# Kernel optimization log

Measured on AMD Instinct MI355X. Metric: run time of the kernel, lower is better.

Reference implementation:

```python
import jax, jax.numpy as jnp
import numpy as np

N_IMG, C, H_IMG, W_IMG = 6, 64, 224, 400
D_RES, H_RES, W_RES = 8, 128, 128
VOXEL = 0.4


def setup_inputs() -> dict:
    key = jax.random.key(0)
    k1, k2, k3, k4 = jax.random.split(key, 4)
    images = jax.random.normal(k1, (N_IMG, C, H_IMG, W_IMG), jnp.float32)
    fx = 0.5 * W_IMG
    K = jnp.array([[fx, 0.0, W_IMG / 2.0], [0.0, fx, H_IMG / 2.0], [0.0, 0.0, 1.0]], jnp.float32)
    intrinsic = K[None] + 0.5 * jax.random.normal(k2, (N_IMG, 3, 3), jnp.float32)
    rotation = jnp.eye(3, dtype=jnp.float32)[None] + 0.05 * jax.random.normal(k3, (N_IMG, 3, 3), jnp.float32)
    translation = 2.0 * jax.random.normal(k4, (N_IMG, 3), jnp.float32) + jnp.array([0.0, 0.0, 5.0], jnp.float32)
    return {"images": images, "intrinsic": intrinsic, "rotation": rotation,
            "translation": translation, "D": D_RES, "H": H_RES, "W": W_RES, "voxelsize": VOXEL}


def _forward(images, intrinsic, rotation, translation, D, H, W, voxelsize):
    N, Cc, Hi, Wi = images.shape
    # voxel-center grid, built exactly like torch.meshgrid(x,y,z) (ij indexing) -> [H,W,D,3]
    x = jnp.arange(H, dtype=jnp.float32) - (H - 1) / 2.0
    y = jnp.arange(W, dtype=jnp.float32) - (W - 1) / 2.0
    z = jnp.arange(D, dtype=jnp.float32) - (D - 1) / 2.0
    gx, gy, gz = jnp.meshgrid(x, y, z, indexing='ij')
    pts = jnp.stack([gx, gy, gz], axis=-1).reshape(-1, 3) * voxelsize  # [P, 3], P = H*W*D
    # lidar -> camera -> pixel (grid @ R^T + t, then @ K^T)
    cam = jnp.einsum('pj,nij->npi', pts, rotation) + translation[:, None, :]  # [N, P, 3]
    pix = jnp.einsum('npj,nij->npi', cam, intrinsic)                          # [N, P, 3]
    mask = pix[..., 2] < 0.1                                                  # [N, P]
    uv = pix[..., :2] / pix[..., 2:3]                                         # (u, v)
    g = uv[..., ::-1]                                                         # flip(-1) -> (v, u)
    scale = jnp.array([Hi - 1, Wi - 1], jnp.float32)
    g = 2.0 * g / scale - 1.0                                                 # normalized grid [N, P, 2]
    # torch grid_sample: bilinear, padding_mode='zeros', align_corners=False
    xs = ((g[..., 0] + 1.0) * Wi - 1.0) / 2.0   # grid x -> width axis
    ys = ((g[..., 1] + 1.0) * Hi - 1.0) / 2.0   # grid y -> height axis
    # clip far-out-of-range coords to keep weights finite; in-range math unchanged
    xs = jnp.clip(xs, -10.0, Wi + 10.0)
    ys = jnp.clip(ys, -10.0, Hi + 10.0)
    x0 = jnp.floor(xs)
    y0 = jnp.floor(ys)
    wx = xs - x0  # frac weights
    wy = ys - y0
    x0i = x0.astype(jnp.int32)
    y0i = y0.astype(jnp.int32)
    flat = images.reshape(N, Cc, Hi * Wi)

    def gather(ix, iy):  # ix, iy [N, P] -> [N, C, P], zeros outside image
        inr = (ix >= 0) & (ix < Wi) & (iy >= 0) & (iy < Hi)
        idx = jnp.clip(iy, 0, Hi - 1) * Wi + jnp.clip(ix, 0, Wi - 1)
        v = jax.vmap(lambda im, i: im[:, i])(flat, idx)  # [N, C, P]
        return jnp.where(inr[:, None, :], v, 0.0)

    v00 = gather(x0i, y0i)
    v10 = gather(x0i + 1, y0i)
    v01 = gather(x0i, y0i + 1)
    v11 = gather(x0i + 1, y0i + 1)
    wxe = wx[:, None, :]
    wye = wy[:, None, :]
    sampled = (v00 * (1 - wxe) * (1 - wye) + v10 * wxe * (1 - wye)
               + v01 * (1 - wxe) * wye + v11 * wxe * wye)        # [N, C, P]
    sampled = jnp.where(mask[:, None, :], 0.0, sampled)          # masked_fill
    return sampled.mean(axis=0).reshape(Cc, D, H, W)


def reference(images, intrinsic, rotation, translation, D, H, W, voxelsize):
    return _forward(images, intrinsic, rotation, translation, D, H, W, voxelsize)
```

## Files before the change

kernel.cpp:

```cpp
#include <hip/hip_runtime.h>
#include <hip/hip_fp16.h>


#define N_IMG 6
#define C_CH  64
#define HI    224
#define WI    400
#define HW    (HI * WI)
#define D_RES 8
#define H_RES 128
#define W_RES 128
#define P_TOT (D_RES * H_RES * W_RES)
#define VOX   0.4f
#define ROWH2 (WI * 32)

__global__ __launch_bounds__(256) void transpose_k(const float* __restrict__ in,
                                                   __half* __restrict__ outh) {
    __shared__ float tile[64 * 65];
    int b      = blockIdx.x;
    int n      = b / 1400;
    int s_base = (b % 1400) * 64;
    int t    = threadIdx.x;
    int col4 = t & 15;
    int crow = t >> 4;

    const float* inp = in + (size_t)n * C_CH * HW + s_base;
#pragma unroll
    for (int i = 0; i < 4; ++i) {
        int c = i * 16 + crow;
        const float4 v = *(const float4*)(inp + (size_t)c * HW + 4 * col4);
        tile[c * 65 + 4 * col4 + 0] = v.x;
        tile[c * 65 + 4 * col4 + 1] = v.y;
        tile[c * 65 + 4 * col4 + 2] = v.z;
        tile[c * 65 + 4 * col4 + 3] = v.w;
    }
    __syncthreads();

    struct __align__(8) H4 { __half2 a, b; };
    int ch4 = 4 * (t & 15);
    H4* outp = (H4*)outh;
#pragma unroll
    for (int i = 0; i < 4; ++i) {
        int pix = i * 16 + (t >> 4);
        H4 pk;
        pk.a = __floats2half2_rn(tile[(ch4 + 0) * 65 + pix],
                                 tile[(ch4 + 1) * 65 + pix]);
        pk.b = __floats2half2_rn(tile[(ch4 + 2) * 65 + pix],
                                 tile[(ch4 + 3) * 65 + pix]);
        outp[(size_t)(n * HW + s_base + pix) * 16 + (ch4 >> 2)] = pk;
    }
}

__device__ __forceinline__ void make_rec(int p, int n,
                                         const float* __restrict__ Kmat,
                                         const float* __restrict__ Rmat,
                                         const float* __restrict__ Tvec,
                                         float4& wout, int& oout) {
#pragma clang fp contract(off)
    int ih = p >> 10;
    int iw = (p >> 3) & (W_RES - 1);
    int id = p & (D_RES - 1);

    float px = ((float)ih - 63.5f) * VOX;
    float py = ((float)iw - 63.5f) * VOX;
    float pz = ((float)id - 3.5f) * VOX;

    const float* R = Rmat + n * 9;
    const float* K = Kmat + n * 9;
    const float* T = Tvec + n * 3;

    float cx = px * R[0] + py * R[1] + pz * R[2] + T[0];
    float cy = px * R[3] + py * R[4] + pz * R[5] + T[1];
    float cz = px * R[6] + py * R[7] + pz * R[8] + T[2];

    float pix0 = cx * K[0] + cy * K[1] + cz * K[2];
    float pix1 = cx * K[3] + cy * K[4] + cz * K[5];
    float pix2 = cx * K[6] + cy * K[7] + cz * K[8];

    if (pix2 < 0.1f) {
        wout = make_float4(0.0f, 0.0f, 0.0f, 0.0f);
        oout = n * (HW * 32);
        return;
    }
    float u = pix0 / pix2;
    float v = pix1 / pix2;
    float g0 = 2.0f * v / 223.0f - 1.0f;
    float g1 = 2.0f * u / 399.0f - 1.0f;
    float xs = ((g0 + 1.0f) * 400.0f - 1.0f) * 0.5f;
    float ys = ((g1 + 1.0f) * 224.0f - 1.0f) * 0.5f;
    xs = fminf(fmaxf(xs, -10.0f), 410.0f);
    ys = fminf(fmaxf(ys, -10.0f), 234.0f);
    float x0f = floorf(xs), y0f = floorf(ys);
    float wx = xs - x0f, wy = ys - y0f;
    int x0 = (int)x0f, y0 = (int)y0f;
    int x1 = x0 + 1, y1 = y0 + 1;

    int bx = min(max(x0, 0), WI - 2);
    int by = min(max(y0, 0), HI - 2);
    float wxA = (bx     == x0) ? (1.0f - wx) : ((bx     == x1) ? wx : 0.0f);
    float wxB = (bx + 1 == x0) ? (1.0f - wx) : ((bx + 1 == x1) ? wx : 0.0f);
    float wyA = (by     == y0) ? (1.0f - wy) : ((by     == y1) ? wy : 0.0f);
    float wyB = (by + 1 == y0) ? (1.0f - wy) : ((by + 1 == y1) ? wy : 0.0f);

    const float inv6 = 1.0f / 6.0f;
    wout.x = wxA * wyA * inv6;
    wout.y = wxB * wyA * inv6;
    wout.z = wxA * wyB * inv6;
    wout.w = wxB * wyB * inv6;
    oout = n * (HW * 32) + (by * WI + bx) * 32;
}

__global__ __launch_bounds__(256) void sample_k(const float* __restrict__ Kmat,
                                                const float* __restrict__ Rmat,
                                                const float* __restrict__ Tvec,
                                                const __half2* __restrict__ imgT2,
                                                float* __restrict__ out) {
    __shared__ float4 swt4[64 * N_IMG];
    __shared__ int    sof[64 * N_IMG];
    __shared__ float  sout[64 * 66];

    int t = threadIdx.x;
    int bid    = ((blockIdx.x & 7) << 8) | (blockIdx.x >> 3);
    int p_base = bid * 64;

    for (int i = t; i < 64 * N_IMG; i += 256) {
        float4 w; int o;
        make_rec(p_base + i / N_IMG, i % N_IMG, Kmat, Rmat, Tvec, w, o);
        swt4[i] = w;
        sof[i]  = o;
    }
    __syncthreads();

    int lane = t & 63;
    int wv   = t >> 6;
    int k    = lane & 31;
    int row  = lane >> 5;
    int sel  = row * 2 + (k >> 4);

    struct __align__(8) H2X2 { __half2 a, b; };
    const float*   swtF    = (const float*)swt4;
    const __half2* rowbase = imgT2 + row * ROWH2 + 2 * k;

#pragma unroll 4
    for (int j = 0; j < 16; ++j) {
        int pl = wv * 16 + j;
        float4 acc = make_float4(0.0f, 0.0f, 0.0f, 0.0f);
#pragma unroll
        for (int n = 0; n < N_IMG; ++n) {
            int   rec = pl * N_IMG + n;
            float w   = swtF[rec * 4 + sel];
            int   o   = sof[rec];
            const H2X2 v = *(const H2X2*)(rowbase + o);
            float2 lo = __half22float2(v.a);
            float2 hi = __half22float2(v.b);
            acc.x = fmaf(w, lo.x, acc.x);
            acc.y = fmaf(w, lo.y, acc.y);
            acc.z = fmaf(w, hi.x, acc.z);
            acc.w = fmaf(w, hi.y, acc.w);
        }
        acc.x += __shfl_xor(acc.x, 32, 64);
        acc.y += __shfl_xor(acc.y, 32, 64);
        acc.z += __shfl_xor(acc.z, 32, 64);
        acc.w += __shfl_xor(acc.w, 32, 64);
        acc.x += __shfl_xor(acc.x, 16, 64);
        acc.y += __shfl_xor(acc.y, 16, 64);
        acc.z += __shfl_xor(acc.z, 16, 64);
        acc.w += __shfl_xor(acc.w, 16, 64);
        if (lane < 16) {
            *(float2*)&sout[pl * 66 + 4 * lane]     = make_float2(acc.x, acc.y);
            *(float2*)&sout[pl * 66 + 4 * lane + 2] = make_float2(acc.z, acc.w);
        }
    }
    __syncthreads();

    int csub = t >> 6;
#pragma unroll
    for (int i = 0; i < 16; ++i) {
        int c = csub * 16 + i;
        __builtin_nontemporal_store(sout[lane * 66 + c],
                                    &out[(size_t)c * P_TOT + p_base + lane]);
    }
}

extern "C" void kernel_launch(void* const* d_in, const int* in_sizes, int n_in,
                              void* d_out, int out_size, void* d_ws, size_t ws_size,
                              hipStream_t stream) {
    const float* images = (const float*)d_in[0];
    const float* intr   = (const float*)d_in[1];
    const float* rot    = (const float*)d_in[2];
    const float* trans  = (const float*)d_in[3];

    __half* imgT = (__half*)d_ws;
    float*  outp = (float*)d_out;

    transpose_k<<<N_IMG * (HW / 64), 256, 0, stream>>>(images, imgT);
    sample_k<<<P_TOT / 64, 256, 0, stream>>>(intr, rot, trans,
                                             (const __half2*)imgT, outp);
}
```

Before: 259.9 us.

## Widen transpose tiles, convert to half before LDS, add XOR swizzle and XCD remap

The transpose kernel now handles 256 pixels per block instead of 64. It converts fp32 to half while loading and stores packed half4 into a 32 KB LDS tile with an XOR swizzle in place of padding. The write-out unpacks pairs of pixels into two 64-bit stores, and block IDs are remapped so each XCD gets a contiguous chunk. The goal is to cut LDS traffic and bank conflicts and improve the locality of global reads and writes in the preprocessing pass. The cost is more LDS per block, which can lower occupancy, plus extra bit manipulation.

```diff
diff --git a/kernel.cpp b/kernel.cpp
--- a/kernel.cpp
+++ b/kernel.cpp
@@ -14,40 +14,60 @@
 #define VOX   0.4f
 #define ROWH2 (WI * 32)
 
+#define TPPB  256
+#define NTILE (HW / TPPB)
+#define NTB   (N_IMG * NTILE)
+
 __global__ __launch_bounds__(256) void transpose_k(const float* __restrict__ in,
                                                    __half* __restrict__ outh) {
-    __shared__ float tile[64 * 65];
-    int b      = blockIdx.x;
-    int n      = b / 1400;
-    int s_base = (b % 1400) * 64;
-    int t    = threadIdx.x;
-    int col4 = t & 15;
-    int crow = t >> 4;
+    __shared__ unsigned int tile32[64 * 128];
+    struct __align__(8) H4 { __half2 a, b; };
+
+    const int q = NTB / 8, r = NTB % 8;
+    int xcd = blockIdx.x & 7, idx = blockIdx.x >> 3;
+    int bid = (xcd < r) ? xcd * (q + 1) + idx
+                        : r * (q + 1) + (xcd - r) * q + idx;
+
+    int n      = bid / NTILE;
+    int s_base = (bid % NTILE) * TPPB;
+    int t = threadIdx.x;
+    int w = t >> 6, l = t & 63;
 
     const float* inp = in + (size_t)n * C_CH * HW + s_base;
-#pragma unroll
-    for (int i = 0; i < 4; ++i) {
-        int c = i * 16 + crow;
-        const float4 v = *(const float4*)(inp + (size_t)c * HW + 4 * col4);
-        tile[c * 65 + 4 * col4 + 0] = v.x;
-        tile[c * 65 + 4 * col4 + 1] = v.y;
-        tile[c * 65 + 4 * col4 + 2] = v.z;
-        tile[c * 65 + 4 * col4 + 3] = v.w;
+    H4* tl8 = (H4*)tile32;
+#pragma unroll
+    for (int i = 0; i < 16; ++i) {
+        int c = w * 16 + i;
+        const float4 v = *(const float4*)(inp + (size_t)c * HW + 4 * l);
+        H4 pk;
+        pk.a = __floats2half2_rn(v.x, v.y);
+        pk.b = __floats2half2_rn(v.z, v.w);
+        tl8[c * 64 + (l ^ ((c >> 2) & 7))] = pk;
     }
     __syncthreads();
 
-    struct __align__(8) H4 { __half2 a, b; };
-    int ch4 = 4 * (t & 15);
-    H4* outp = (H4*)outh;
-#pragma unroll
-    for (int i = 0; i < 4; ++i) {
-        int pix = i * 16 + (t >> 4);
-        H4 pk;
-        pk.a = __floats2half2_rn(tile[(ch4 + 0) * 65 + pix],
-                                 tile[(ch4 + 1) * 65 + pix]);
-        pk.b = __floats2half2_rn(tile[(ch4 + 2) * 65 + pix],
-                                 tile[(ch4 + 3) * 65 + pix]);
-        outp[(size_t)(n * HW + s_base + pix) * 16 + (ch4 >> 2)] = pk;
+    int cq = t & 15;
+    int hc = cq & 7;
+    unsigned long long* o64 = (unsigned long long*)outh;
+#pragma unroll
+    for (int pass = 0; pass < 8; ++pass) {
+        int pp = pass * 16 + (t >> 4);
+        int gd = 2 * ((pp >> 1) ^ hc) + (pp & 1);
+        unsigned int q0 = tile32[(4 * cq + 0) * 128 + gd];
+        unsigned int q1 = tile32[(4 * cq + 1) * 128 + gd];
+        unsigned int q2 = tile32[(4 * cq + 2) * 128 + gd];
+        unsigned int q3 = tile32[(4 * cq + 3) * 128 + gd];
+        unsigned long long e = (unsigned long long)(q0 & 0xffffu)
+                             | ((unsigned long long)(q1 & 0xffffu) << 16)
+                             | ((unsigned long long)(q2 & 0xffffu) << 32)
+                             | ((unsigned long long)(q3 & 0xffffu) << 48);
+        unsigned long long o = (unsigned long long)(q0 >> 16)
+                             | ((unsigned long long)(q1 >> 16) << 16)
+                             | ((unsigned long long)(q2 >> 16) << 32)
+                             | ((unsigned long long)(q3 >> 16) << 48);
+        size_t base = (size_t)(n * HW + s_base + 2 * pp) * 16 + cq;
+        o64[base]      = e;
+        o64[base + 16] = o;
     }
 }
 
@@ -193,7 +213,7 @@
     __half* imgT = (__half*)d_ws;
     float*  outp = (float*)d_out;
 
-    transpose_k<<<N_IMG * (HW / 64), 256, 0, stream>>>(images, imgT);
+    transpose_k<<<NTB, 256, 0, stream>>>(images, imgT);
     sample_k<<<P_TOT / 64, 256, 0, stream>>>(intr, rot, trans,
                                              (const __half2*)imgT, outp);
 }
```

Result: no change. 263.4 us (+1.4%).
